# Kernel optimization log

Measured on AMD Instinct MI355X. Metric: run time of the kernel, lower is better.

## Reference

```python
import jax, jax.numpy as jnp
import numpy as np

B, S, D, H, HS = 4, 2048, 1024, 16, 64
DFF = 4 * D
EPS = 1e-5


def setup_inputs() -> dict:
    key = jax.random.key(0)
    ks = jax.random.split(key, 16)
    std = 0.02
    return {
        "x": jax.random.normal(ks[0], (B, S, D), jnp.float32),
        "Wq": jax.random.normal(ks[1], (H, D, HS), jnp.float32) * std,
        "bq": jnp.zeros((H, HS), jnp.float32),
        "Wk": jax.random.normal(ks[2], (H, D, HS), jnp.float32) * std,
        "bk": jnp.zeros((H, HS), jnp.float32),
        "Wv": jax.random.normal(ks[3], (H, D, HS), jnp.float32) * std,
        "bv": jnp.zeros((H, HS), jnp.float32),
        "Wp": jax.random.normal(ks[4], (D, D), jnp.float32) * std,
        "bp": jnp.zeros((D,), jnp.float32),
        "ln1_w": jnp.ones((D,), jnp.float32),
        "ln1_b": jnp.zeros((D,), jnp.float32),
        "ln2_w": jnp.ones((D,), jnp.float32),
        "ln2_b": jnp.zeros((D,), jnp.float32),
        "W1": jax.random.normal(ks[5], (D, DFF), jnp.float32) * std,
        "b1": jnp.zeros((DFF,), jnp.float32),
        "W2": jax.random.normal(ks[6], (DFF, D), jnp.float32) * std,
        "b2": jnp.zeros((D,), jnp.float32),
    }


def _layernorm(x, w, b):
    mu = jnp.mean(x, axis=-1, keepdims=True)
    var = jnp.mean(jnp.square(x - mu), axis=-1, keepdims=True)
    return (x - mu) * jax.lax.rsqrt(var + EPS) * w + b


def _block(x, Wq, bq, Wk, bk, Wv, bv, Wp, bp, ln1_w, ln1_b, ln2_w, ln2_b, W1, b1, W2, b2):
    seq = x.shape[1]
    xn = _layernorm(x, ln1_w, ln1_b)
    # batched per-head projections: [B,H,S,HS]
    q = jnp.einsum('bsd,hdk->bhsk', xn, Wq) + bq[:, None, :]
    k = jnp.einsum('bsd,hdk->bhsk', xn, Wk) + bk[:, None, :]
    v = jnp.einsum('bsd,hdk->bhsk', xn, Wv) + bv[:, None, :]
    scores = jnp.einsum('bhsk,bhtk->bhst', q, k)
    mask = jnp.tril(jnp.ones((seq, seq), bool))
    # original: masked_fill(-inf) then divide by sqrt(head_size) -> equivalent
    scores = jnp.where(mask, scores / jnp.sqrt(jnp.float32(HS)), -jnp.inf)
    attn = jax.nn.softmax(scores, axis=-1)
    out = jnp.einsum('bhst,bhtk->bhsk', attn, v)
    out = out.transpose(0, 2, 1, 3).reshape(x.shape[0], seq, H * HS)
    att = out @ Wp + bp
    x = x + att
    xn2 = _layernorm(x, ln2_w, ln2_b)
    h = jax.nn.gelu(xn2 @ W1 + b1, approximate=False)  # torch nn.GELU default = exact
    ffn = h @ W2 + b2
    return x + ffn


def reference(x, Wq, bq, Wk, bk, Wv, bv, Wp, bp, ln1_w, ln1_b, ln2_w, ln2_b, W1, b1, W2, b2):
    out = _block(x, Wq, bq, Wk, bk, Wv, bv, Wp, bp, ln1_w, ln1_b, ln2_w, ln2_b, W1, b1, W2, b2)
    return out
```

## Files before the change

kernel.cpp:

```cpp
#include <hip/hip_runtime.h>
#include <hip/hip_bf16.h>

#define D_MODEL 1024
#define SEQ 2048
#define NH 16
#define HSZ 64
#define DFF_ 4096

typedef __attribute__((ext_vector_type(8))) short short8;
typedef __attribute__((ext_vector_type(4))) short short4v;
typedef __attribute__((ext_vector_type(4))) float f32x4;

static __device__ __forceinline__ short f2bf(float f) {
  unsigned u = __builtin_bit_cast(unsigned, f);
  u = u + 0x7fffu + ((u >> 16) & 1u);
  return (short)(u >> 16);
}

static __device__ __forceinline__ unsigned packbf2(float a, float b) {
  return (unsigned)(unsigned short)f2bf(a) | ((unsigned)(unsigned short)f2bf(b) << 16);
}

static __device__ __forceinline__ f32x4 mfma16(short8 a, short8 b, f32x4 c) {
  return __builtin_amdgcn_mfma_f32_16x16x32_bf16(a, b, c, 0, 0, 0);
}

static __device__ __forceinline__ void gld16(const short* g, short* l) {
  __builtin_amdgcn_global_load_lds((const __attribute__((address_space(1))) void*)g,
                                   (__attribute__((address_space(3))) void*)l, 16, 0, 0);
}

__global__ void transpose_qkv_kernel(const float* __restrict__ Wq, const float* __restrict__ Wk,
                                     const float* __restrict__ Wv, short* __restrict__ dst) {
  __shared__ float tile[32][33];
  const int z = blockIdx.z;
  const int which = z >> 4, hh = z & 15;
  const float* src = (which == 0 ? Wq : which == 1 ? Wk : Wv) + (long)hh * (D_MODEL * HSZ);
  const int c0 = blockIdx.x * 32, r0 = blockIdx.y * 32;
  const int tx = threadIdx.x, ty = threadIdx.y;
#pragma unroll
  for (int i = 0; i < 4; ++i)
    tile[ty + 8 * i][tx] = src[(long)(r0 + ty + 8 * i) * HSZ + c0 + tx];
  __syncthreads();
#pragma unroll
  for (int i = 0; i < 4; ++i)
    dst[((long)which * 1024 + hh * 64 + c0 + ty + 8 * i) * D_MODEL + r0 + tx] =
        f2bf(tile[tx][ty + 8 * i]);
}

__global__ void transpose_gen_kernel(const float* __restrict__ src, short* __restrict__ dst,
                                     int R, int C) {
  __shared__ float tile[32][33];
  const int c0 = blockIdx.x * 32, r0 = blockIdx.y * 32;
  const int tx = threadIdx.x, ty = threadIdx.y;
#pragma unroll
  for (int i = 0; i < 4; ++i)
    tile[ty + 8 * i][tx] = src[(long)(r0 + ty + 8 * i) * C + c0 + tx];
  __syncthreads();
#pragma unroll
  for (int i = 0; i < 4; ++i)
    dst[(long)(c0 + ty + 8 * i) * R + r0 + tx] = f2bf(tile[tx][ty + 8 * i]);
}

__global__ void v_transpose_kernel(const short* __restrict__ vb, short* __restrict__ vt) {
  __shared__ short tile[64 * 72];
  const int bh = blockIdx.y;
  const int t0 = blockIdx.x * 64;
  const long base = (long)bh * SEQ * HSZ;
  const int tid = threadIdx.x;
  const int r = tid >> 3, c = (tid & 7) * 8;
#pragma unroll
  for (int it = 0; it < 2; ++it) {
    const int rr = r + it * 32;
    *(short8*)&tile[rr * 72 + c] = *(const short8*)(vb + base + (long)(t0 + rr) * HSZ + c);
  }
  __syncthreads();
#pragma unroll
  for (int it = 0; it < 2; ++it) {
    const int rr = r + it * 32;
    short8 o;
#pragma unroll
    for (int u = 0; u < 8; ++u) o[u] = tile[(c + u) * 72 + rr];
    *(short8*)(vt + base + (long)rr * SEQ + t0 + c) = o;
  }
}

__global__ void ln_kernel(const float* __restrict__ x, const float* __restrict__ w,
                          const float* __restrict__ b, short* __restrict__ out) {
  const int row = blockIdx.x;
  const float* xr = x + (size_t)row * D_MODEL;
  const int t = threadIdx.x;
  float4 v = *(const float4*)(xr + t * 4);
  float s = v.x + v.y + v.z + v.w;
  float s2 = v.x * v.x + v.y * v.y + v.z * v.z + v.w * v.w;
#pragma unroll
  for (int o = 1; o < 64; o <<= 1) {
    s += __shfl_xor(s, o, 64);
    s2 += __shfl_xor(s2, o, 64);
  }
  __shared__ float ps[8];
  const int lane = t & 63, wid = t >> 6;
  if (lane == 0) { ps[wid] = s; ps[wid + 4] = s2; }
  __syncthreads();
  s = ps[0] + ps[1] + ps[2] + ps[3];
  s2 = ps[4] + ps[5] + ps[6] + ps[7];
  const float mu = s * (1.0f / D_MODEL);
  const float var = s2 * (1.0f / D_MODEL) - mu * mu;
  const float rs = rsqrtf(var + 1e-5f);
  float4 wv = *(const float4*)(w + t * 4);
  float4 bv = *(const float4*)(b + t * 4);
  short4v o4;
  o4[0] = f2bf((v.x - mu) * rs * wv.x + bv.x);
  o4[1] = f2bf((v.y - mu) * rs * wv.y + bv.y);
  o4[2] = f2bf((v.z - mu) * rs * wv.z + bv.z);
  o4[3] = f2bf((v.w - mu) * rs * wv.w + bv.w);
  *(short4v*)(out + (size_t)row * D_MODEL + t * 4) = o4;
}

template <int MODE, int TM>
__global__ __launch_bounds__(512, 2) void gemm_kernel(
    const short* __restrict__ A, const short* __restrict__ Bt, const int K,
    const float* __restrict__ c0, const float* __restrict__ c1,
    const float* __restrict__ c2, const float* __restrict__ res,
    void* __restrict__ o0, void* __restrict__ o1, void* __restrict__ o2) {
  constexpr int MF = TM / 32;
  constexpr int NA = TM / 64;
  constexpr int NS = NA + 4;
  __shared__ short As[2][TM * 64];
  __shared__ short Bs[2][256 * 64];
  const int tid = threadIdx.x;
  const int lane = tid & 63, wid = tid >> 6;
  const int wm = wid >> 2, wn = wid & 3;
  const int l16 = lane & 15, lg = lane >> 4;
  const long r0 = (long)blockIdx.y * TM;
  const long n0 = (long)blockIdx.x * 256;

  long offA[NA], offB[4];
#pragma unroll
  for (int i = 0; i < NA; ++i) {
    const int o = wid * 64 + lane + i * 512;
    const int row = o >> 3, slot = o & 7;
    offA[i] = (long)(r0 + row) * K + ((slot ^ (row & 7)) << 3);
  }
#pragma unroll
  for (int i = 0; i < 4; ++i) {
    const int o = wid * 64 + lane + i * 512;
    const int row = o >> 3, slot = o & 7;
    offB[i] = (long)(n0 + row) * K + ((slot ^ (row & 7)) << 3);
  }

  f32x4 acc[MF][4];
#pragma unroll
  for (int m = 0; m < MF; ++m)
#pragma unroll
    for (int n = 0; n < 4; ++n) {
      f32x4 z = {0.f, 0.f, 0.f, 0.f};
      acc[m][n] = z;
    }

  const int x7 = l16 & 7;
  const int psl0 = (lg ^ x7) * 8, psl1 = ((4 + lg) ^ x7) * 8;
  const int aBase = (wm * (TM / 2) + l16) * 64;
  const int bBase = (wn * 64 + l16) * 64;

  const int NT = K >> 6;
#pragma unroll
  for (int i = 0; i < NA; ++i) gld16(A + offA[i], &As[0][(wid * 64 + i * 512) * 8]);
#pragma unroll
  for (int i = 0; i < 4; ++i) gld16(Bt + offB[i], &Bs[0][(wid * 64 + i * 512) * 8]);
  __syncthreads();

  for (int t = 0; t < NT; ++t) {
    const int cur = t & 1;
    const int kt = t << 6;
    const short* Ac = As[cur];
    const short* Bc = Bs[cur];
    const bool hasnext = (t + 1 < NT);
    short8 bfr[4][2];
#pragma unroll
    for (int n = 0; n < 4; ++n) {
      bfr[n][0] = *(const short8*)&Bc[bBase + n * 1024 + psl0];
      bfr[n][1] = *(const short8*)&Bc[bBase + n * 1024 + psl1];
    }
#pragma unroll
    for (int m = 0; m < MF; ++m) {
      if (hasnext) {
        const int s0 = (m * NS) / MF, s1 = ((m + 1) * NS) / MF;
#pragma unroll
        for (int s = s0; s < s1; ++s) {
          if (s < NA)
            gld16(A + offA[s] + kt + 64, &As[cur ^ 1][(wid * 64 + s * 512) * 8]);
          else
            gld16(Bt + offB[s - NA] + kt + 64,
                  &Bs[cur ^ 1][(wid * 64 + (s - NA) * 512) * 8]);
        }
      }
      const short8 a0 = *(const short8*)&Ac[aBase + m * 1024 + psl0];
      const short8 a1 = *(const short8*)&Ac[aBase + m * 1024 + psl1];
      __builtin_amdgcn_s_setprio(1);
#pragma unroll
      for (int n = 0; n < 4; ++n) {
        acc[m][n] = mfma16(a0, bfr[n][0], acc[m][n]);
        acc[m][n] = mfma16(a1, bfr[n][1], acc[m][n]);
      }
      __builtin_amdgcn_s_setprio(0);
    }
    __syncthreads();
  }

#pragma unroll
  for (int m = 0; m < MF; ++m) {
    const long rowb = r0 + wm * (TM / 2) + m * 16 + lg * 4;
#pragma unroll
    for (int n = 0; n < 4; ++n) {
      const long col = n0 + wn * 64 + n * 16 + l16;
#pragma unroll
      for (int j = 0; j < 4; ++j) {
        float val = acc[m][n][j];
        const long rr = rowb + j;
        if (MODE == 0) {
          const int c10 = (int)col & 1023;
          const int which = (int)col >> 10;
          const float* bb = which == 0 ? c0 : which == 1 ? c1 : c2;
          short* oo = (short*)(which == 0 ? o0 : which == 1 ? o1 : o2);
          val += bb[c10];
          const long bidx = rr >> 11, sidx = rr & 2047;
          const int h = c10 >> 6, hs = c10 & 63;
          oo[(((bidx * NH) + h) * SEQ + sidx) * HSZ + hs] = f2bf(val);
        } else if (MODE == 1) {
          val += c0[col] + res[rr * D_MODEL + col];
          ((float*)o0)[rr * D_MODEL + col] = val;
        } else if (MODE == 2) {
          val += c0[col];
          const float g = 0.5f * val * (1.0f + erff(val * 0.70710678118654752f));
          ((short*)o0)[rr * DFF_ + col] = f2bf(g);
        } else {
          val += c0[col] + res[rr * D_MODEL + col];
          ((float*)o0)[rr * D_MODEL + col] = val;
        }
      }
    }
  }
}

#define SM_SCALE 0.18033688011112042f

__global__ void attn_kernel(const short* __restrict__ q, const short* __restrict__ k,
                            const short* __restrict__ vt, short* __restrict__ att) {
  const int qt = (SEQ / 128 - 1) - (int)blockIdx.y;
  const int bh = blockIdx.x;
  const int b = bh >> 4, h = bh & 15;
  const int tid = threadIdx.x;
  const int lane = tid & 63, wq = tid >> 6;
  const int l16 = lane & 15, lg = lane >> 4;
  const long base = (long)bh * SEQ * HSZ;

  __shared__ short Ks[64 * 64];
  __shared__ short Vts[64 * 64];
  __shared__ short Ps[4 * 32 * 72];
  short* Psw = &Ps[wq * 32 * 72];

  const int R0 = qt * 128 + wq * 32;

  short8 qf[2][2];
#pragma unroll
  for (int qn = 0; qn < 2; ++qn)
#pragma unroll
    for (int kk = 0; kk < 2; ++kk)
      qf[qn][kk] =
          *(const short8*)(q + base + (long)(R0 + qn * 16 + l16) * HSZ + kk * 32 + lg * 8);

  float m_[2] = {-INFINITY, -INFINITY};
  float l_[2] = {0.f, 0.f};
  f32x4 oacc[2][4];
#pragma unroll
  for (int qn = 0; qn < 2; ++qn)
#pragma unroll
    for (int hf = 0; hf < 4; ++hf) {
      f32x4 z = {0.f, 0.f, 0.f, 0.f};
      oacc[qn][hf] = z;
    }

  const int srow = tid >> 3, wg = tid & 7;
  const int swc = (wg ^ (srow & 7)) * 8;
  const int x7 = l16 & 7;
  const int rc0 = (lg ^ x7) * 8, rc1 = ((4 + lg) ^ x7) * 8;
  const int tend = (qt + 1) * 128;

  for (int t0 = 0; t0 < tend; t0 += 64) {
    __syncthreads();
#pragma unroll
    for (int it = 0; it < 2; ++it) {
      const int r = srow + it * 32;
      const short8 kv = *(const short8*)(k + base + (long)(t0 + r) * HSZ + wg * 8);
      const short8 vv = *(const short8*)(vt + base + (long)r * SEQ + t0 + wg * 8);
      *(short8*)&Ks[r * 64 + swc] = kv;
      *(short8*)&Vts[r * 64 + swc] = vv;
    }
    __syncthreads();

    if (t0 <= R0 + 31) {
      f32x4 sf[4][2];
#pragma unroll
      for (int tt = 0; tt < 4; ++tt)
#pragma unroll
        for (int qn = 0; qn < 2; ++qn) {
          f32x4 z = {0.f, 0.f, 0.f, 0.f};
          sf[tt][qn] = z;
        }
      __builtin_amdgcn_s_setprio(1);
#pragma unroll
      for (int kk = 0; kk < 2; ++kk)
#pragma unroll
        for (int tt = 0; tt < 4; ++tt) {
          short8 kf = *(const short8*)&Ks[(tt * 16 + l16) * 64 + (kk ? rc1 : rc0)];
#pragma unroll
          for (int qn = 0; qn < 2; ++qn) sf[tt][qn] = mfma16(kf, qf[qn][kk], sf[tt][qn]);
        }
      __builtin_amdgcn_s_setprio(0);

      const bool domask = (t0 + 63 > R0);
      const int tb = t0 + lg * 4;
#pragma unroll
      for (int tt = 0; tt < 4; ++tt)
#pragma unroll
        for (int qn = 0; qn < 2; ++qn) {
          const int qg = R0 + qn * 16 + l16;
#pragma unroll
          for (int j = 0; j < 4; ++j) {
            float s = sf[tt][qn][j] * SM_SCALE;
            if (domask && (tb + tt * 16 + j > qg)) s = -INFINITY;
            sf[tt][qn][j] = s;
          }
        }

      float mx[2];
#pragma unroll
      for (int qn = 0; qn < 2; ++qn) {
        float m0 = sf[0][qn][0];
#pragma unroll
        for (int tt = 0; tt < 4; ++tt)
#pragma unroll
          for (int j = 0; j < 4; ++j) m0 = fmaxf(m0, sf[tt][qn][j]);
        m0 = fmaxf(m0, __shfl_xor(m0, 16, 64));
        m0 = fmaxf(m0, __shfl_xor(m0, 32, 64));
        mx[qn] = m0;
      }
      const int ok = (mx[0] <= m_[0] + 8.f) && (mx[1] <= m_[1] + 8.f);
      if (!__all(ok)) {
#pragma unroll
        for (int qn = 0; qn < 2; ++qn) {
          const float mnew = fmaxf(m_[qn], mx[qn]);
          const float rc = exp2f(m_[qn] - mnew);
          m_[qn] = mnew;
          l_[qn] *= rc;
#pragma unroll
          for (int hf = 0; hf < 4; ++hf)
#pragma unroll
            for (int j = 0; j < 4; ++j) oacc[qn][hf][j] *= rc;
        }
      }
#pragma unroll
      for (int qn = 0; qn < 2; ++qn) {
        float sum = 0.f;
#pragma unroll
        for (int tt = 0; tt < 4; ++tt)
#pragma unroll
          for (int j = 0; j < 4; ++j) {
            const float p = exp2f(sf[tt][qn][j] - m_[qn]);
            sf[tt][qn][j] = p;
            sum += p;
          }
        l_[qn] += sum;
      }

#pragma unroll
      for (int qn = 0; qn < 2; ++qn)
#pragma unroll
        for (int tt = 0; tt < 4; ++tt) {
          const int ro = (qn * 16 + l16) * 72 + tt * 16 + lg * 4;
          *(unsigned*)&Psw[ro] = packbf2(sf[tt][qn][0], sf[tt][qn][1]);
          *(unsigned*)&Psw[ro + 2] = packbf2(sf[tt][qn][2], sf[tt][qn][3]);
        }

      __builtin_amdgcn_s_setprio(1);
#pragma unroll
      for (int kk = 0; kk < 2; ++kk) {
        short8 pa[2];
#pragma unroll
        for (int qn = 0; qn < 2; ++qn)
          pa[qn] = *(const short8*)&Psw[(qn * 16 + l16) * 72 + kk * 32 + lg * 8];
#pragma unroll
        for (int hf = 0; hf < 4; ++hf) {
          short8 vf = *(const short8*)&Vts[(hf * 16 + l16) * 64 + (kk ? rc1 : rc0)];
#pragma unroll
          for (int qn = 0; qn < 2; ++qn)
            oacc[qn][hf] = mfma16(vf, pa[qn], oacc[qn][hf]);
        }
      }
      __builtin_amdgcn_s_setprio(0);
    }
  }

#pragma unroll
  for (int qn = 0; qn < 2; ++qn) {
    float lt = l_[qn];
    lt += __shfl_xor(lt, 16, 64);
    lt += __shfl_xor(lt, 32, 64);
    const float inv = 1.0f / lt;
    const long row = R0 + qn * 16 + l16;
#pragma unroll
    for (int hf = 0; hf < 4; ++hf) {
      short4v o4;
#pragma unroll
      for (int j = 0; j < 4; ++j) o4[j] = f2bf(oacc[qn][hf][j] * inv);
      *(short4v*)(att + ((long)b * SEQ + row) * D_MODEL + h * HSZ + hf * 16 + lg * 4) = o4;
    }
  }
}

extern "C" void kernel_launch(void* const* d_in, const int* in_sizes, int n_in,
                              void* d_out, int out_size, void* d_ws, size_t ws_size,
                              hipStream_t stream) {
  const float* x = (const float*)d_in[0];
  const float* Wq = (const float*)d_in[1];
  const float* bq = (const float*)d_in[2];
  const float* Wk = (const float*)d_in[3];
  const float* bk = (const float*)d_in[4];
  const float* Wv = (const float*)d_in[5];
  const float* bv = (const float*)d_in[6];
  const float* Wp = (const float*)d_in[7];
  const float* bp = (const float*)d_in[8];
  const float* g1 = (const float*)d_in[9];
  const float* be1 = (const float*)d_in[10];
  const float* g2 = (const float*)d_in[11];
  const float* be2 = (const float*)d_in[12];
  const float* W1 = (const float*)d_in[13];
  const float* b1 = (const float*)d_in[14];
  const float* W2 = (const float*)d_in[15];
  const float* b2 = (const float*)d_in[16];
  float* out = (float*)d_out;
  char* ws = (char*)d_ws;

  if (ws_size < 209715200ull) return;

  short* WqkvT = (short*)(ws + 0);
  short* WpT = (short*)(ws + 6291456);
  short* W1T = (short*)(ws + 8388608);
  short* W2T = (short*)(ws + 16777216);
  short* xn = (short*)(ws + 25165824);
  short* vt = (short*)(ws + 25165824);
  short* qb = (short*)(ws + 41943040);
  short* kb = (short*)(ws + 58720256);
  short* vb = (short*)(ws + 75497472);
  short* att = (short*)(ws + 92274688);
  float* x1 = (float*)(ws + 109051904);
  short* hb = (short*)(ws + 142606336);

  dim3 tb(32, 8);
  transpose_qkv_kernel<<<dim3(2, 32, 48), tb, 0, stream>>>(Wq, Wk, Wv, WqkvT);
  transpose_gen_kernel<<<dim3(32, 32), tb, 0, stream>>>(Wp, WpT, 1024, 1024);
  transpose_gen_kernel<<<dim3(128, 32), tb, 0, stream>>>(W1, W1T, 1024, 4096);
  transpose_gen_kernel<<<dim3(32, 128), tb, 0, stream>>>(W2, W2T, 4096, 1024);
  ln_kernel<<<8192, 256, 0, stream>>>(x, g1, be1, xn);
  gemm_kernel<0, 256><<<dim3(12, 32), 512, 0, stream>>>(xn, WqkvT, 1024, bq, bk, bv,
                                                        nullptr, qb, kb, vb);
  v_transpose_kernel<<<dim3(32, 64), 256, 0, stream>>>(vb, vt);
  attn_kernel<<<dim3(64, 16), 256, 0, stream>>>(qb, kb, vt, att);
  gemm_kernel<1, 128><<<dim3(4, 64), 512, 0, stream>>>(att, WpT, 1024, bp, nullptr,
                                                       nullptr, x, x1, nullptr, nullptr);
  ln_kernel<<<8192, 256, 0, stream>>>(x1, g2, be2, xn);
  gemm_kernel<2, 256><<<dim3(16, 32), 512, 0, stream>>>(xn, W1T, 1024, b1, nullptr,
                                                        nullptr, nullptr, hb, nullptr,
                                                        nullptr);
  gemm_kernel<3, 128><<<dim3(4, 64), 512, 0, stream>>>(hb, W2T, 4096, b2, nullptr,
                                                       nullptr, x1, out, nullptr, nullptr);
}
```

Before: 486.9 us.

## Unify GEMMs on 128x256 tiles with XCD-aware block remapping and quadrant fragment loads

Every GEMM now uses a fixed 128x256 tile. Previously the QKV and W1 GEMMs used 256-row tiles. Launches become 1D grids whose block IDs are remapped so that consecutive tiles land on the same XCD (bid&7 interleave), which should improve L2 reuse. The inner loop issues all next-tile prefetches up front and loads A/B fragments per 2x2 quadrant instead of keeping all B fragments live, which lowers register pressure. The trade-off is that smaller tiles for the large GEMMs mean more blocks and more redundant B loads, and global-load interleaving with the MFMAs is lost.

```diff
diff --git a/kernel.cpp b/kernel.cpp
--- a/kernel.cpp
+++ b/kernel.cpp
@@ -117,41 +117,42 @@
   *(short4v*)(out + (size_t)row * D_MODEL + t * 4) = o4;
 }
 
-template <int MODE, int TM>
+template <int MODE>
 __global__ __launch_bounds__(512, 2) void gemm_kernel(
     const short* __restrict__ A, const short* __restrict__ Bt, const int K,
-    const float* __restrict__ c0, const float* __restrict__ c1,
+    const int gridX, const float* __restrict__ c0, const float* __restrict__ c1,
     const float* __restrict__ c2, const float* __restrict__ res,
     void* __restrict__ o0, void* __restrict__ o1, void* __restrict__ o2) {
-  constexpr int MF = TM / 32;
-  constexpr int NA = TM / 64;
-  constexpr int NS = NA + 4;
-  __shared__ short As[2][TM * 64];
+  __shared__ short As[2][128 * 64];
   __shared__ short Bs[2][256 * 64];
+  const int nwg = (int)gridDim.x;
+  const int bid0 = (int)blockIdx.x;
+  const int bid = (bid0 & 7) * (nwg >> 3) + (bid0 >> 3);
+  const int bx = bid % gridX, by = bid / gridX;
+  const long r0 = (long)by * 128;
+  const long n0 = (long)bx * 256;
   const int tid = threadIdx.x;
   const int lane = tid & 63, wid = tid >> 6;
   const int wm = wid >> 2, wn = wid & 3;
   const int l16 = lane & 15, lg = lane >> 4;
-  const long r0 = (long)blockIdx.y * TM;
-  const long n0 = (long)blockIdx.x * 256;
-
-  long offA[NA], offB[4];
-#pragma unroll
-  for (int i = 0; i < NA; ++i) {
-    const int o = wid * 64 + lane + i * 512;
-    const int row = o >> 3, slot = o & 7;
+
+  long offA[2], offB[4];
+#pragma unroll
+  for (int i = 0; i < 2; ++i) {
+    const int c = tid + i * 512;
+    const int row = c >> 3, slot = c & 7;
     offA[i] = (long)(r0 + row) * K + ((slot ^ (row & 7)) << 3);
   }
 #pragma unroll
   for (int i = 0; i < 4; ++i) {
-    const int o = wid * 64 + lane + i * 512;
-    const int row = o >> 3, slot = o & 7;
+    const int c = tid + i * 512;
+    const int row = c >> 3, slot = c & 7;
     offB[i] = (long)(n0 + row) * K + ((slot ^ (row & 7)) << 3);
   }
 
-  f32x4 acc[MF][4];
-#pragma unroll
-  for (int m = 0; m < MF; ++m)
+  f32x4 acc[4][4];
+#pragma unroll
+  for (int m = 0; m < 4; ++m)
 #pragma unroll
     for (int n = 0; n < 4; ++n) {
       f32x4 z = {0.f, 0.f, 0.f, 0.f};
@@ -159,58 +160,61 @@
     }
 
   const int x7 = l16 & 7;
-  const int psl0 = (lg ^ x7) * 8, psl1 = ((4 + lg) ^ x7) * 8;
-  const int aBase = (wm * (TM / 2) + l16) * 64;
-  const int bBase = (wn * 64 + l16) * 64;
+  const int sw0 = (lg ^ x7) * 8, sw1 = ((4 + lg) ^ x7) * 8;
+
+#define STAGE_T(kt, buf)                                                      \
+  {                                                                           \
+    _Pragma("unroll") for (int i = 0; i < 2; ++i)                             \
+        gld16(A + offA[i] + (kt), &As[buf][(tid + i * 512) * 8]);             \
+    _Pragma("unroll") for (int i = 0; i < 4; ++i)                             \
+        gld16(Bt + offB[i] + (kt), &Bs[buf][(tid + i * 512) * 8]);            \
+  }
 
   const int NT = K >> 6;
-#pragma unroll
-  for (int i = 0; i < NA; ++i) gld16(A + offA[i], &As[0][(wid * 64 + i * 512) * 8]);
-#pragma unroll
-  for (int i = 0; i < 4; ++i) gld16(Bt + offB[i], &Bs[0][(wid * 64 + i * 512) * 8]);
+  STAGE_T(0, 0);
   __syncthreads();
 
   for (int t = 0; t < NT; ++t) {
-    const int cur = t & 1;
-    const int kt = t << 6;
-    const short* Ac = As[cur];
-    const short* Bc = Bs[cur];
-    const bool hasnext = (t + 1 < NT);
-    short8 bfr[4][2];
-#pragma unroll
-    for (int n = 0; n < 4; ++n) {
-      bfr[n][0] = *(const short8*)&Bc[bBase + n * 1024 + psl0];
-      bfr[n][1] = *(const short8*)&Bc[bBase + n * 1024 + psl1];
-    }
-#pragma unroll
-    for (int m = 0; m < MF; ++m) {
-      if (hasnext) {
-        const int s0 = (m * NS) / MF, s1 = ((m + 1) * NS) / MF;
-#pragma unroll
-        for (int s = s0; s < s1; ++s) {
-          if (s < NA)
-            gld16(A + offA[s] + kt + 64, &As[cur ^ 1][(wid * 64 + s * 512) * 8]);
-          else
-            gld16(Bt + offB[s - NA] + kt + 64,
-                  &Bs[cur ^ 1][(wid * 64 + (s - NA) * 512) * 8]);
-        }
-      }
-      const short8 a0 = *(const short8*)&Ac[aBase + m * 1024 + psl0];
-      const short8 a1 = *(const short8*)&Ac[aBase + m * 1024 + psl1];
-      __builtin_amdgcn_s_setprio(1);
-#pragma unroll
-      for (int n = 0; n < 4; ++n) {
-        acc[m][n] = mfma16(a0, bfr[n][0], acc[m][n]);
-        acc[m][n] = mfma16(a1, bfr[n][1], acc[m][n]);
-      }
-      __builtin_amdgcn_s_setprio(0);
-    }
+    const int p = t & 1;
+    if (t + 1 < NT) STAGE_T((t + 1) << 6, p ^ 1);
+    const short* Ap = As[p];
+    const short* Bp = Bs[p];
+#pragma unroll
+    for (int mq = 0; mq < 2; ++mq)
+#pragma unroll
+      for (int nq = 0; nq < 2; ++nq) {
+        short8 af[2][2], bf[2][2];
+#pragma unroll
+        for (int m = 0; m < 2; ++m) {
+          const int r = wm * 64 + mq * 32 + m * 16 + l16;
+          af[m][0] = *(const short8*)&Ap[r * 64 + sw0];
+          af[m][1] = *(const short8*)&Ap[r * 64 + sw1];
+        }
+#pragma unroll
+        for (int n = 0; n < 2; ++n) {
+          const int r = wn * 64 + nq * 32 + n * 16 + l16;
+          bf[n][0] = *(const short8*)&Bp[r * 64 + sw0];
+          bf[n][1] = *(const short8*)&Bp[r * 64 + sw1];
+        }
+        __builtin_amdgcn_s_setprio(1);
+#pragma unroll
+        for (int m = 0; m < 2; ++m)
+#pragma unroll
+          for (int n = 0; n < 2; ++n) {
+            acc[mq * 2 + m][nq * 2 + n] =
+                mfma16(af[m][0], bf[n][0], acc[mq * 2 + m][nq * 2 + n]);
+            acc[mq * 2 + m][nq * 2 + n] =
+                mfma16(af[m][1], bf[n][1], acc[mq * 2 + m][nq * 2 + n]);
+          }
+        __builtin_amdgcn_s_setprio(0);
+      }
     __syncthreads();
   }
-
-#pragma unroll
-  for (int m = 0; m < MF; ++m) {
-    const long rowb = r0 + wm * (TM / 2) + m * 16 + lg * 4;
+#undef STAGE_T
+
+#pragma unroll
+  for (int m = 0; m < 4; ++m) {
+    const long rowb = r0 + wm * 64 + m * 16 + lg * 4;
 #pragma unroll
     for (int n = 0; n < 4; ++n) {
       const long col = n0 + wn * 64 + n * 16 + l16;
@@ -463,16 +467,15 @@
   transpose_gen_kernel<<<dim3(128, 32), tb, 0, stream>>>(W1, W1T, 1024, 4096);
   transpose_gen_kernel<<<dim3(32, 128), tb, 0, stream>>>(W2, W2T, 4096, 1024);
   ln_kernel<<<8192, 256, 0, stream>>>(x, g1, be1, xn);
-  gemm_kernel<0, 256><<<dim3(12, 32), 512, 0, stream>>>(xn, WqkvT, 1024, bq, bk, bv,
-                                                        nullptr, qb, kb, vb);
+  gemm_kernel<0><<<768, 512, 0, stream>>>(xn, WqkvT, 1024, 12, bq, bk, bv, nullptr, qb,
+                                          kb, vb);
   v_transpose_kernel<<<dim3(32, 64), 256, 0, stream>>>(vb, vt);
   attn_kernel<<<dim3(64, 16), 256, 0, stream>>>(qb, kb, vt, att);
-  gemm_kernel<1, 128><<<dim3(4, 64), 512, 0, stream>>>(att, WpT, 1024, bp, nullptr,
-                                                       nullptr, x, x1, nullptr, nullptr);
+  gemm_kernel<1><<<256, 512, 0, stream>>>(att, WpT, 1024, 4, bp, nullptr, nullptr, x, x1,
+                                          nullptr, nullptr);
   ln_kernel<<<8192, 256, 0, stream>>>(x1, g2, be2, xn);
-  gemm_kernel<2, 256><<<dim3(16, 32), 512, 0, stream>>>(xn, W1T, 1024, b1, nullptr,
-                                                        nullptr, nullptr, hb, nullptr,
-                                                        nullptr);
-  gemm_kernel<3, 128><<<dim3(4, 64), 512, 0, stream>>>(hb, W2T, 4096, b2, nullptr,
-                                                       nullptr, x1, out, nullptr, nullptr);
-}
+  gemm_kernel<2><<<1024, 512, 0, stream>>>(xn, W1T, 1024, 16, b1, nullptr, nullptr,
+                                           nullptr, hb, nullptr, nullptr);
+  gemm_kernel<3><<<256, 512, 0, stream>>>(hb, W2T, 4096, 4, b2, nullptr, nullptr, x1, out,
+                                          nullptr, nullptr);
+}
```

Measured after the change: 481.7 us. About the same (-1.1%).

## Restructure GEMM main loop into phased pipeline with fine-grained vmcnt waits

Applied to the files above, without the earlier changes.

The GEMM K-loop is split into phases. Each phase loads its A fragments from LDS, issues a slice of the next tile's global-to-LDS copies, and uses explicit s_waitcnt vmcnt counts with raw barriers instead of a full __syncthreads per tile. The A tile row mapping is permuted so each phase reads a contiguous LDS chunk. Separately, the softmax scale is folded into Q in the QKV GEMM epilogue, so attention only applies the causal mask on diagonal tiles, and the QKV GEMM switches from 256-row to 128-row tiles. The hand-tuned wait counts are fragile and add barrier traffic.

```diff
diff --git a/kernel.cpp b/kernel.cpp
--- a/kernel.cpp
+++ b/kernel.cpp
@@ -29,6 +29,9 @@
   __builtin_amdgcn_global_load_lds((const __attribute__((address_space(1))) void*)g,
                                    (__attribute__((address_space(3))) void*)l, 16, 0, 0);
 }
+
+#define SM_SCALE 0.18033688011112042f
+#define VMW(n) asm volatile("s_waitcnt vmcnt(" #n ")" ::: "memory")
 
 __global__ void transpose_qkv_kernel(const float* __restrict__ Wq, const float* __restrict__ Wk,
                                      const float* __restrict__ Wv, short* __restrict__ dst) {
@@ -117,41 +120,45 @@
   *(short4v*)(out + (size_t)row * D_MODEL + t * 4) = o4;
 }
 
-template <int MODE, int TM>
+template <int MODE, int BM>
 __global__ __launch_bounds__(512, 2) void gemm_kernel(
     const short* __restrict__ A, const short* __restrict__ Bt, const int K,
     const float* __restrict__ c0, const float* __restrict__ c1,
     const float* __restrict__ c2, const float* __restrict__ res,
     void* __restrict__ o0, void* __restrict__ o1, void* __restrict__ o2) {
-  constexpr int MF = TM / 32;
-  constexpr int NA = TM / 64;
-  constexpr int NS = NA + 4;
-  __shared__ short As[2][TM * 64];
+  constexpr int NPH = BM / 64;
+  constexpr int NA = BM / 64;
+  constexpr int NTOT = NA + 4;
+  constexpr int PER = NTOT / NPH;
+  constexpr int HM = BM / 2;
+  __shared__ short As[2][BM * 64];
   __shared__ short Bs[2][256 * 64];
+  const long r0 = (long)blockIdx.y * BM;
+  const long n0 = (long)blockIdx.x * 256;
   const int tid = threadIdx.x;
   const int lane = tid & 63, wid = tid >> 6;
   const int wm = wid >> 2, wn = wid & 3;
   const int l16 = lane & 15, lg = lane >> 4;
-  const long r0 = (long)blockIdx.y * TM;
-  const long n0 = (long)blockIdx.x * 256;
 
   long offA[NA], offB[4];
 #pragma unroll
   for (int i = 0; i < NA; ++i) {
-    const int o = wid * 64 + lane + i * 512;
-    const int row = o >> 3, slot = o & 7;
-    offA[i] = (long)(r0 + row) * K + ((slot ^ (row & 7)) << 3);
+    const int c = tid + i * 512;
+    const int lam = c >> 3, s = c & 7;
+    const int cch = lam >> 6, rho = lam & 63;
+    const int g = cch * 32 + (rho & 31) + ((rho >> 5) ? HM : 0);
+    offA[i] = (long)(r0 + g) * K + ((s ^ (lam & 7)) << 3);
   }
 #pragma unroll
   for (int i = 0; i < 4; ++i) {
-    const int o = wid * 64 + lane + i * 512;
-    const int row = o >> 3, slot = o & 7;
-    offB[i] = (long)(n0 + row) * K + ((slot ^ (row & 7)) << 3);
-  }
-
-  f32x4 acc[MF][4];
-#pragma unroll
-  for (int m = 0; m < MF; ++m)
+    const int c = tid + i * 512;
+    const int row = c >> 3, s = c & 7;
+    offB[i] = (long)(n0 + row) * K + ((s ^ (row & 7)) << 3);
+  }
+
+  f32x4 acc[2 * NPH][4];
+#pragma unroll
+  for (int m = 0; m < 2 * NPH; ++m)
 #pragma unroll
     for (int n = 0; n < 4; ++n) {
       f32x4 z = {0.f, 0.f, 0.f, 0.f};
@@ -159,58 +166,77 @@
     }
 
   const int x7 = l16 & 7;
-  const int psl0 = (lg ^ x7) * 8, psl1 = ((4 + lg) ^ x7) * 8;
-  const int aBase = (wm * (TM / 2) + l16) * 64;
-  const int bBase = (wn * 64 + l16) * 64;
+  const int sw0 = (lg ^ x7) * 8, sw1 = ((4 + lg) ^ x7) * 8;
+
+#define STG(j, kt, buf)                                                      \
+  {                                                                          \
+    if ((j) < 4)                                                             \
+      gld16(Bt + offB[(j)] + (kt), &Bs[buf][(tid + (j)*512) * 8]);           \
+    else                                                                     \
+      gld16(A + offA[(j)-4] + (kt), &As[buf][(tid + ((j)-4) * 512) * 8]);    \
+  }
+
+#define GPHASE(P, ENDSTMT)                                                   \
+  {                                                                          \
+    short8 af[2][2];                                                         \
+    _Pragma("unroll") for (int mm = 0; mm < 2; ++mm) {                       \
+      const int lam = (P)*64 + wm * 32 + mm * 16 + l16;                      \
+      af[mm][0] = *(const short8*)&Ap[lam * 64 + sw0];                       \
+      af[mm][1] = *(const short8*)&Ap[lam * 64 + sw1];                       \
+    }                                                                        \
+    if ((P) == 0) {                                                          \
+      _Pragma("unroll") for (int n = 0; n < 4; ++n) {                        \
+        const int r = (wn * 64 + n * 16 + l16) * 64;                         \
+        bf[n][0] = *(const short8*)&Bp[r + sw0];                             \
+        bf[n][1] = *(const short8*)&Bp[r + sw1];                             \
+      }                                                                      \
+    }                                                                        \
+    if (st) {                                                                \
+      _Pragma("unroll") for (int j = (P)*PER; j < ((P) + 1) * PER; ++j)      \
+          STG(j, ktn, nb);                                                   \
+    }                                                                        \
+    __builtin_amdgcn_s_barrier();                                            \
+    asm volatile("s_waitcnt lgkmcnt(0)" ::: "memory");                       \
+    __builtin_amdgcn_sched_barrier(0);                                       \
+    __builtin_amdgcn_s_setprio(1);                                           \
+    _Pragma("unroll") for (int kk = 0; kk < 2; ++kk)                         \
+        _Pragma("unroll") for (int mm = 0; mm < 2; ++mm)                     \
+        _Pragma("unroll") for (int n = 0; n < 4; ++n) acc[2 * (P) + mm][n] = \
+        mfma16(af[mm][kk], bf[n][kk], acc[2 * (P) + mm][n]);                 \
+    __builtin_amdgcn_s_setprio(0);                                           \
+    ENDSTMT;                                                                 \
+    __builtin_amdgcn_s_barrier();                                            \
+  }
 
   const int NT = K >> 6;
 #pragma unroll
-  for (int i = 0; i < NA; ++i) gld16(A + offA[i], &As[0][(wid * 64 + i * 512) * 8]);
-#pragma unroll
-  for (int i = 0; i < 4; ++i) gld16(Bt + offB[i], &Bs[0][(wid * 64 + i * 512) * 8]);
-  __syncthreads();
+  for (int j = 0; j < NTOT; ++j) STG(j, 0, 0);
+  if constexpr (BM == 256) VMW(3); else VMW(1);
+  __builtin_amdgcn_s_barrier();
 
   for (int t = 0; t < NT; ++t) {
-    const int cur = t & 1;
-    const int kt = t << 6;
-    const short* Ac = As[cur];
-    const short* Bc = Bs[cur];
-    const bool hasnext = (t + 1 < NT);
-    short8 bfr[4][2];
-#pragma unroll
-    for (int n = 0; n < 4; ++n) {
-      bfr[n][0] = *(const short8*)&Bc[bBase + n * 1024 + psl0];
-      bfr[n][1] = *(const short8*)&Bc[bBase + n * 1024 + psl1];
-    }
-#pragma unroll
-    for (int m = 0; m < MF; ++m) {
-      if (hasnext) {
-        const int s0 = (m * NS) / MF, s1 = ((m + 1) * NS) / MF;
-#pragma unroll
-        for (int s = s0; s < s1; ++s) {
-          if (s < NA)
-            gld16(A + offA[s] + kt + 64, &As[cur ^ 1][(wid * 64 + s * 512) * 8]);
-          else
-            gld16(Bt + offB[s - NA] + kt + 64,
-                  &Bs[cur ^ 1][(wid * 64 + (s - NA) * 512) * 8]);
-        }
-      }
-      const short8 a0 = *(const short8*)&Ac[aBase + m * 1024 + psl0];
-      const short8 a1 = *(const short8*)&Ac[aBase + m * 1024 + psl1];
-      __builtin_amdgcn_s_setprio(1);
-#pragma unroll
-      for (int n = 0; n < 4; ++n) {
-        acc[m][n] = mfma16(a0, bfr[n][0], acc[m][n]);
-        acc[m][n] = mfma16(a1, bfr[n][1], acc[m][n]);
-      }
-      __builtin_amdgcn_s_setprio(0);
-    }
-    __syncthreads();
-  }
-
-#pragma unroll
-  for (int m = 0; m < MF; ++m) {
-    const long rowb = r0 + wm * (TM / 2) + m * 16 + lg * 4;
+    const int cur = t & 1, nb = cur ^ 1;
+    const short* Ap = As[cur];
+    const short* Bp = Bs[cur];
+    const bool st = (t + 1 < NT);
+    const int ktn = (t + 1) << 6;
+    short8 bf[4][2];
+    if constexpr (BM == 256) {
+      GPHASE(0, { if (st) VMW(4); else VMW(2); });
+      GPHASE(1, { if (st) VMW(5); else VMW(1); });
+      GPHASE(2, { if (st) VMW(6); else VMW(0); });
+      GPHASE(3, { if (st) VMW(3); });
+    } else {
+      GPHASE(0, { if (st) VMW(3); else VMW(0); });
+      GPHASE(1, { if (st) VMW(1); });
+    }
+  }
+#undef GPHASE
+#undef STG
+
+#pragma unroll
+  for (int m = 0; m < 2 * NPH; ++m) {
+    const long rowb = r0 + wm * HM + m * 16 + lg * 4;
 #pragma unroll
     for (int n = 0; n < 4; ++n) {
       const long col = n0 + wn * 64 + n * 16 + l16;
@@ -224,6 +250,7 @@
           const float* bb = which == 0 ? c0 : which == 1 ? c1 : c2;
           short* oo = (short*)(which == 0 ? o0 : which == 1 ? o1 : o2);
           val += bb[c10];
+          if (which == 0) val *= SM_SCALE;
           const long bidx = rr >> 11, sidx = rr & 2047;
           const int h = c10 >> 6, hs = c10 & 63;
           oo[(((bidx * NH) + h) * SEQ + sidx) * HSZ + hs] = f2bf(val);
@@ -243,8 +270,6 @@
   }
 }
 
-#define SM_SCALE 0.18033688011112042f
-
 __global__ void attn_kernel(const short* __restrict__ q, const short* __restrict__ k,
                             const short* __restrict__ vt, short* __restrict__ att) {
   const int qt = (SEQ / 128 - 1) - (int)blockIdx.y;
@@ -320,19 +345,18 @@
       __builtin_amdgcn_s_setprio(0);
 
       const bool domask = (t0 + 63 > R0);
-      const int tb = t0 + lg * 4;
-#pragma unroll
-      for (int tt = 0; tt < 4; ++tt)
-#pragma unroll
-        for (int qn = 0; qn < 2; ++qn) {
-          const int qg = R0 + qn * 16 + l16;
-#pragma unroll
-          for (int j = 0; j < 4; ++j) {
-            float s = sf[tt][qn][j] * SM_SCALE;
-            if (domask && (tb + tt * 16 + j > qg)) s = -INFINITY;
-            sf[tt][qn][j] = s;
+      if (domask) {
+        const int tb = t0 + lg * 4;
+#pragma unroll
+        for (int tt = 0; tt < 4; ++tt)
+#pragma unroll
+          for (int qn = 0; qn < 2; ++qn) {
+            const int qg = R0 + qn * 16 + l16;
+#pragma unroll
+            for (int j = 0; j < 4; ++j)
+              if (tb + tt * 16 + j > qg) sf[tt][qn][j] = -INFINITY;
           }
-        }
+      }
 
       float mx[2];
 #pragma unroll
@@ -463,7 +487,7 @@
   transpose_gen_kernel<<<dim3(128, 32), tb, 0, stream>>>(W1, W1T, 1024, 4096);
   transpose_gen_kernel<<<dim3(32, 128), tb, 0, stream>>>(W2, W2T, 4096, 1024);
   ln_kernel<<<8192, 256, 0, stream>>>(x, g1, be1, xn);
-  gemm_kernel<0, 256><<<dim3(12, 32), 512, 0, stream>>>(xn, WqkvT, 1024, bq, bk, bv,
+  gemm_kernel<0, 128><<<dim3(12, 64), 512, 0, stream>>>(xn, WqkvT, 1024, bq, bk, bv,
                                                         nullptr, qb, kb, vb);
   v_transpose_kernel<<<dim3(32, 64), 256, 0, stream>>>(vb, vt);
   attn_kernel<<<dim3(64, 16), 256, 0, stream>>>(qb, kb, vt, att);
```

Measured after the change: 414.8 us, median of 2. 14.8% less time.
